# Performance work log

Hardware: AMD Instinct MI355X
Metric: run time of the kernel (lower is better)

## Reference

```python
import math
import jax, jax.numpy as jnp
import numpy as np

LN_EPS = 1e-5
SIG_DOMAIN = 5.0


def _layer_norm(x, gamma, beta):
    mu = jnp.mean(x, axis=-1, keepdims=True)
    var = jnp.var(x, axis=-1, keepdims=True)
    return (x - mu) / jnp.sqrt(var + LN_EPS) * gamma + beta


def setup_inputs() -> dict:
    key = jax.random.key(0)
    k0, k1, k2, k3 = jax.random.split(key, 4)
    B, H, S, D = 4, 16, 1024, 256   # batch, c_heads, seq, input_dim
    A, O = 128, 256                 # attention_dim, output_dim
    x = jax.random.normal(k0, (B, H, S, D), dtype=jnp.float32)
    # torch.rand -> uniform [0,1)
    W_query = jax.random.uniform(k1, (H, A, D), dtype=jnp.float32)
    W_key = jax.random.uniform(k2, (H, A, D), dtype=jnp.float32)
    W_value = jax.random.uniform(k3, (H, O, D), dtype=jnp.float32)
    gamma = jnp.ones((D,), dtype=jnp.float32)
    beta = jnp.zeros((D,), dtype=jnp.float32)
    return {"x": x, "W_query": W_query, "W_key": W_key, "W_value": W_value,
            "gamma": gamma, "beta": beta}


def reference(x, W_query, W_key, W_value, gamma, beta):
    scale = math.sqrt(x.shape[-1])  # sqrt(input_dim)
    xn = _layer_norm(x, gamma, beta)                       # [B,H,S,D]
    q = jnp.einsum('bhsd,had->bhsa', xn, W_query)          # [B,H,S,A]
    k = jnp.einsum('bhsd,had->bhsa', xn, W_key)            # [B,H,S,A]
    v = jnp.einsum('bhsd,hod->bhso', xn, W_value)          # [B,H,S,O]
    scores = jnp.einsum('bhsa,bhta->bhst', q, k) / scale   # [B,H,S,S]
    # overtaking-sigmoid-tuned normalization
    s_max = jnp.max(scores, axis=-1, keepdims=True)
    s_min = jnp.min(scores, axis=-1, keepdims=True)
    s_norm = (scores - s_min) / (s_max - s_min)
    softmax_sel = 1.0 - jax.nn.sigmoid(
        (1.0 - jnp.max(s_norm, axis=-1, keepdims=True)) * 2.0 * SIG_DOMAIN + SIG_DOMAIN)
    sigmoid_sel = 1.0 - softmax_sel
    weights = (softmax_sel * jax.nn.softmax(s_norm, axis=-1)
               + sigmoid_sel * jax.nn.sigmoid(s_norm * 2.0 * SIG_DOMAIN - SIG_DOMAIN))
    return jnp.einsum('bhst,bhto->bhso', weights, v)       # [B,H,S,O]
```

## Files before the change

### kernel.cpp

```cpp
#include <hip/hip_runtime.h>

typedef __attribute__((ext_vector_type(8))) short bf16x8;
typedef __attribute__((ext_vector_type(8))) _Float16 h16x8;
typedef __attribute__((ext_vector_type(2))) _Float16 h16x2;
typedef __attribute__((ext_vector_type(2))) __fp16 fp16x2;
typedef __attribute__((ext_vector_type(4))) float f32x4;
typedef __attribute__((ext_vector_type(4))) unsigned short us4;
typedef unsigned short u16;

#define MFMA16  __builtin_amdgcn_mfma_f32_16x16x32_bf16
#define MFMA16H __builtin_amdgcn_mfma_f32_16x16x32_f16

__device__ __forceinline__ u16 f2bf(float f) {
  union { float f; unsigned u; } v; v.f = f;
  unsigned r = v.u + 0x7FFFu + ((v.u >> 16) & 1u);
  return (u16)(r >> 16);
}

__device__ __forceinline__ float ex2(float x) {
#if __has_builtin(__builtin_amdgcn_exp2f)
  return __builtin_amdgcn_exp2f(x);
#else
  return exp2f(x);
#endif
}

__device__ __forceinline__ h16x8 sigmoid8(h16x8 sv, float am, float bm) {
  h16x8 pa;
  h16x2* pw = (h16x2*)&pa;
  #pragma unroll
  for (int q = 0; q < 4; q++) {
    float e0 = ex2(fmaf((float)sv[2*q],     am, bm));
    float e1 = ex2(fmaf((float)sv[2*q + 1], am, bm));
    fp16x2 pk = __builtin_amdgcn_cvt_pkrtz(__builtin_amdgcn_rcpf(1.0f + e0),
                                           __builtin_amdgcn_rcpf(1.0f + e1));
    pw[q] = __builtin_bit_cast(h16x2, pk);
  }
  return pa;
}

__global__ __launch_bounds__(256) void ln_kernel(const float* __restrict__ x,
    const float* __restrict__ gamma, const float* __restrict__ beta,
    u16* __restrict__ xn)
{
  int row = blockIdx.x * 4 + (threadIdx.x >> 6);
  int lane = threadIdx.x & 63;
  const float* xr = x + (size_t)row * 256;
  f32x4 v = *(const f32x4*)(xr + lane * 4);
  float s  = v[0] + v[1] + v[2] + v[3];
  float s2 = v[0]*v[0] + v[1]*v[1] + v[2]*v[2] + v[3]*v[3];
  #pragma unroll
  for (int off = 1; off < 64; off <<= 1) {
    s  += __shfl_xor(s, off);
    s2 += __shfl_xor(s2, off);
  }
  float mu   = s * (1.0f / 256.0f);
  float var  = s2 * (1.0f / 256.0f) - mu * mu;
  float rstd = rsqrtf(var + 1e-5f);
  f32x4 g  = *(const f32x4*)(gamma + lane * 4);
  f32x4 bb = *(const f32x4*)(beta  + lane * 4);
  us4 o;
  #pragma unroll
  for (int j = 0; j < 4; j++) o[j] = f2bf((v[j] - mu) * rstd * g[j] + bb[j]);
  *(us4*)(xn + (size_t)row * 256 + lane * 4) = o;
}

__global__ __launch_bounds__(256) void cvt_kernel(const float* __restrict__ in,
    u16* __restrict__ out, int n4)
{
  int i = blockIdx.x * 256 + threadIdx.x;
  if (i >= n4) return;
  f32x4 v = *(const f32x4*)(in + (size_t)i * 4);
  us4 o;
  #pragma unroll
  for (int j = 0; j < 4; j++) o[j] = f2bf(v[j]);
  *(us4*)(out + (size_t)i * 4) = o;
}

__global__ __launch_bounds__(256) void cvt_qk(const float* __restrict__ in,
    u16* __restrict__ out, int half)
{
  int i = blockIdx.x * 256 + threadIdx.x;
  int e4 = i * 4;
  int h = e4 >> 15;
  int rem = e4 & 32767;
  f32x4 v = *(const f32x4*)(in + e4);
  us4 o;
  #pragma unroll
  for (int j = 0; j < 4; j++) o[j] = f2bf(v[j]);
  *(us4*)(out + (size_t)h * 65536 + half * 32768 + rem) = o;
}

__global__ __launch_bounds__(256) void gemm128(const u16* __restrict__ Ag,
    const u16* __restrict__ Bg, u16* __restrict__ Cg,
    int M, int N, int aHead, int bHead, int outHalf)
{
  constexpr int K = 256;
  __shared__ u16 As[128][128];
  __shared__ u16 Bs[128][128];
  int bh = blockIdx.z;
  int m0 = blockIdx.x * 128, n0 = blockIdx.y * 128;
  const u16* Ab = Ag + (size_t)(aHead ? (bh & 15) : bh) * M * K + (size_t)m0 * K;
  const u16* Bb = Bg + (size_t)(bHead ? (bh & 15) : bh) * N * K + (size_t)n0 * K;
  int tid = threadIdx.x, lane = tid & 63, w = tid >> 6;
  int wm = w >> 1, wn = w & 1;
  int lr = lane & 15, g = lane >> 4;

  f32x4 acc[4][4] = {};
  for (int kc = 0; kc < 2; kc++) {
    if (kc) __syncthreads();
    #pragma unroll
    for (int i = 0; i < 8; i++) {
      int c = tid + 256 * i;
      int r = c >> 4, ch = c & 15;
      int sw = (ch ^ (r & 7)) * 8;
      *(bf16x8*)&As[r][sw] = *(const bf16x8*)(Ab + (size_t)r * K + kc * 128 + ch * 8);
      *(bf16x8*)&Bs[r][sw] = *(const bf16x8*)(Bb + (size_t)r * K + kc * 128 + ch * 8);
    }
    __syncthreads();
    #pragma unroll
    for (int ks = 0; ks < 4; ks++) {
      bf16x8 af[4], bfr[4];
      #pragma unroll
      for (int mf = 0; mf < 4; mf++) {
        int r = wm * 64 + mf * 16 + lr;
        af[mf] = *(const bf16x8*)&As[r][((ks * 4 + g) ^ (r & 7)) * 8];
      }
      #pragma unroll
      for (int nf = 0; nf < 4; nf++) {
        int r = wn * 64 + nf * 16 + lr;
        bfr[nf] = *(const bf16x8*)&Bs[r][((ks * 4 + g) ^ (r & 7)) * 8];
      }
      #pragma unroll
      for (int mf = 0; mf < 4; mf++)
        #pragma unroll
        for (int nf = 0; nf < 4; nf++)
          acc[mf][nf] = MFMA16(af[mf], bfr[nf], acc[mf][nf], 0, 0, 0);
    }
  }
  u16* Cb = Cg + (size_t)bh * M * N;
  #pragma unroll
  for (int mf = 0; mf < 4; mf++)
    #pragma unroll
    for (int nf = 0; nf < 4; nf++)
      #pragma unroll
      for (int i = 0; i < 4; i++) {
        int row = m0 + wm * 64 + mf * 16 + g * 4 + i;
        int col = n0 + wn * 64 + nf * 16 + lr;
        u16 ev;
        if (outHalf) { _Float16 hv = (_Float16)acc[mf][nf][i]; ev = *(u16*)&hv; }
        else ev = f2bf(acc[mf][nf][i]);
        Cb[(size_t)row * N + col] = ev;
      }
}

__global__ __launch_bounds__(256) void score_kernel(
    const u16* __restrict__ QKg, _Float16* __restrict__ Sg, float2* __restrict__ rp, int bh0)
{
  constexpr int S = 1024, LD = 256;
  __shared__ u16 Qs[128][128];
  __shared__ u16 Ks[128][128];
  int bid = blockIdx.x;
  int hl = ((bid >> 6) << 3) | (bid & 7);
  int rb = (bid >> 3) & 7;
  int bh = bh0 + hl;
  int m0 = rb * 128;
  int tid = threadIdx.x, lane = tid & 63, w = tid >> 6;
  int lr = lane & 15, g = lane >> 4;
  const u16* Qb = QKg + ((size_t)bh * S + m0) * LD;
  const u16* Kb = QKg + (size_t)bh * S * LD + 128;

  #pragma unroll
  for (int i = 0; i < 8; i++) {
    int c = tid + 256 * i;
    int r = c >> 4, ch = c & 15;
    *(bf16x8*)&Qs[r][(ch ^ (r & 7)) * 8] = *(const bf16x8*)(Qb + (size_t)r * LD + ch * 8);
    *(bf16x8*)&Ks[r][(ch ^ (r & 7)) * 8] = *(const bf16x8*)(Kb + (size_t)r * LD + ch * 8);
  }
  __syncthreads();

  bf16x8 aq[2][4];
  #pragma unroll
  for (int mf = 0; mf < 2; mf++)
    #pragma unroll
    for (int ks = 0; ks < 4; ks++) {
      int r = w * 32 + mf * 16 + lr;
      aq[mf][ks] = *(const bf16x8*)&Qs[r][((ks * 4 + g) ^ (r & 7)) * 8];
    }

  float rmin[2][4], rmax[2][4];
  #pragma unroll
  for (int mf = 0; mf < 2; mf++)
    #pragma unroll
    for (int i = 0; i < 4; i++) { rmin[mf][i] = 3.0e38f; rmax[mf][i] = -3.0e38f; }

  _Float16* Sb = Sg + (size_t)hl * S * S;
  for (int nc = 0; nc < 8; nc++) {
    bf16x8 kreg[8];
    if (nc < 7) {
      #pragma unroll
      for (int i = 0; i < 8; i++) {
        int c = tid + 256 * i;
        int r = c >> 4, ch = c & 15;
        kreg[i] = *(const bf16x8*)(Kb + (size_t)(128 * (nc + 1) + r) * LD + ch * 8);
      }
    }
    f32x4 acc[2][8] = {};
    #pragma unroll
    for (int ks = 0; ks < 4; ks++) {
      bf16x8 bk[8];
      #pragma unroll
      for (int nf = 0; nf < 8; nf++) {
        int r = nf * 16 + lr;
        bk[nf] = *(const bf16x8*)&Ks[r][((ks * 4 + g) ^ (r & 7)) * 8];
      }
      #pragma unroll
      for (int mf = 0; mf < 2; mf++)
        #pragma unroll
        for (int nf = 0; nf < 8; nf++)
          acc[mf][nf] = MFMA16(aq[mf][ks], bk[nf], acc[mf][nf], 0, 0, 0);
    }
    #pragma unroll
    for (int mf = 0; mf < 2; mf++)
      #pragma unroll
      for (int nf = 0; nf < 8; nf++) {
        int kt = nc * 4 + (nf >> 1);
        int cc = (nf & 1) * 16 + lr;
        #pragma unroll
        for (int i = 0; i < 4; i++) {
          int rowT = w * 32 + mf * 16 + g * 4 + i;
          int rb64 = (m0 + rowT) >> 6;
          int rr = rowT & 63;
          Sb[(size_t)rb64 * 65536 + (size_t)kt * 2048 + rr * 32 + cc] = (_Float16)acc[mf][nf][i];
          rmin[mf][i] = fminf(rmin[mf][i], acc[mf][nf][i]);
          rmax[mf][i] = fmaxf(rmax[mf][i], acc[mf][nf][i]);
        }
      }
    __syncthreads();
    if (nc < 7) {
      #pragma unroll
      for (int i = 0; i < 8; i++) {
        int c = tid + 256 * i;
        int r = c >> 4, ch = c & 15;
        *(bf16x8*)&Ks[r][(ch ^ (r & 7)) * 8] = kreg[i];
      }
    }
    __syncthreads();
  }
  #pragma unroll
  for (int off = 1; off < 16; off <<= 1)
    #pragma unroll
    for (int mf = 0; mf < 2; mf++)
      #pragma unroll
      for (int i = 0; i < 4; i++) {
        rmin[mf][i] = fminf(rmin[mf][i], __shfl_xor(rmin[mf][i], off));
        rmax[mf][i] = fmaxf(rmax[mf][i], __shfl_xor(rmax[mf][i], off));
      }
  if (lr == 0) {
    #pragma unroll
    for (int mf = 0; mf < 2; mf++)
      #pragma unroll
      for (int i = 0; i < 4; i++) {
        int row = m0 + w * 32 + mf * 16 + g * 4 + i;
        float inv = 1.0f / (rmax[mf][i] - rmin[mf][i]);
        rp[(size_t)bh * S + row] = make_float2(10.0f * inv, fmaf(-10.0f * rmin[mf][i], inv, -5.0f));
      }
  }
}

__global__ __launch_bounds__(256, 4) void pv_kernel(
    const _Float16* __restrict__ Sg, const float2* __restrict__ rpG,
    const _Float16* __restrict__ VTg, float* __restrict__ Out, int bh0)
{
  constexpr int S = 1024, OD = 256, PSTR = 40;
  __shared__ _Float16 P_lds[2][64 * PSTR];
  int bid = blockIdx.x;
  int hl = ((bid >> 7) << 3) | (bid & 7);
  int rb = (bid >> 3) & 15;
  int bh = bh0 + hl;
  int m0 = rb * 64;
  int tid = threadIdx.x, lane = tid & 63, w = tid >> 6;
  int lr = lane & 15, g = lane >> 4;
  const _Float16* Vb = VTg + (size_t)bh * OD * S;

  const _Float16* Stile = Sg + (size_t)hl * S * S + (size_t)rb * 65536 + (size_t)tid * 8;

  int r0 = tid >> 2;
  float2 pp = rpG[(size_t)bh * S + m0 + r0];
  float am = -pp.x * 1.44269504f, bm = -pp.y * 1.44269504f;
  _Float16* Pw0 = &P_lds[0][r0 * PSTR + (tid & 3) * 8];
  _Float16* Pw1 = &P_lds[1][r0 * PSTR + (tid & 3) * 8];

  const _Float16* Vrow[4];
  #pragma unroll
  for (int of = 0; of < 4; of++)
    Vrow[of] = Vb + (size_t)(w * 64 + of * 16 + lr) * S + g * 8;

  f32x4 acc[4][4] = {};

  h16x8 sv0 = *(const h16x8*)(Stile);
  h16x8 sv1 = *(const h16x8*)(Stile + 2048);
  h16x8 va[4], vb[4];
  #pragma unroll
  for (int of = 0; of < 4; of++) va[of] = *(const h16x8*)(Vrow[of]);
  *(h16x8*)Pw0 = sigmoid8(sv0, am, bm);
  __syncthreads();

  for (int kt = 0; kt < 32; kt++) {
    int cur = kt & 1;
    if (kt < 31) {
      #pragma unroll
      for (int of = 0; of < 4; of++)
        vb[of] = *(const h16x8*)(Vrow[of] + (kt + 1) * 32);
    }
    h16x8 svn;
    if (kt < 30) svn = *(const h16x8*)(Stile + (size_t)(kt + 2) * 2048);
    if (kt < 31)
      *(h16x8*)(cur ? Pw0 : Pw1) = sigmoid8(sv1, am, bm);
    __builtin_amdgcn_s_setprio(1);
    #pragma unroll
    for (int rf = 0; rf < 4; rf++) {
      h16x8 pb = *(const h16x8*)&P_lds[cur][(rf * 16 + lr) * PSTR + g * 8];
      #pragma unroll
      for (int of = 0; of < 4; of++)
        acc[of][rf] = MFMA16H(va[of], pb, acc[of][rf], 0, 0, 0);
    }
    __builtin_amdgcn_s_setprio(0);
    #pragma unroll
    for (int of = 0; of < 4; of++) va[of] = vb[of];
    sv0 = sv1; sv1 = svn;
    __syncthreads();
  }

  const float c2 = 0.9933071490757153f;
  float* Ob = Out + (size_t)bh * S * OD;
  #pragma unroll
  for (int of = 0; of < 4; of++)
    #pragma unroll
    for (int rf = 0; rf < 4; rf++) {
      f32x4 v = acc[of][rf];
      #pragma unroll
      for (int i = 0; i < 4; i++) v[i] *= c2;
      int row = m0 + rf * 16 + lr;
      int col = w * 64 + of * 16 + g * 4;
      *(f32x4*)(Ob + (size_t)row * OD + col) = v;
    }
}

extern "C" void kernel_launch(void* const* d_in, const int* in_sizes, int n_in,
                              void* d_out, int out_size, void* d_ws, size_t ws_size,
                              hipStream_t stream) {
  const float* x     = (const float*)d_in[0];
  const float* Wq    = (const float*)d_in[1];
  const float* Wk    = (const float*)d_in[2];
  const float* Wv    = (const float*)d_in[3];
  const float* gamma = (const float*)d_in[4];
  const float* beta  = (const float*)d_in[5];
  float* out = (float*)d_out;

  constexpr int B = 4, H = 16, S = 1024, D = 256, A = 128, O = 256;
  constexpr int BH = B * H;

  char* p = (char*)d_ws;
  size_t off = 0;
  auto take = [&](size_t n) { off = (off + 255) & ~(size_t)255; char* q = p + off; off += n; return q; };

  u16*    xn   = (u16*)take((size_t)BH * S * D * 2);
  u16*    qkb  = (u16*)take((size_t)BH * S * 256 * 2);
  u16*    vtb  = (u16*)take((size_t)BH * O * S * 2);
  u16*    wqkb = (u16*)take((size_t)H * 256 * D * 2);
  u16*    wvb  = (u16*)take((size_t)H * O * D * 2);
  float2* rp   = (float2*)take((size_t)BH * S * 8);

  int grp = 1;
  for (; grp < 8; grp <<= 1) {
    size_t need = ((off + 255) & ~(size_t)255) + (size_t)(BH / grp) * S * S * 2;
    if (need <= ws_size) break;
  }
  int hp = BH / grp;
  _Float16* sG = (_Float16*)take((size_t)hp * S * S * 2);

  ln_kernel<<<BH * S / 4, 256, 0, stream>>>(x, gamma, beta, xn);

  cvt_qk<<<(H * A * D / 4) / 256, 256, 0, stream>>>(Wq, wqkb, 0);
  cvt_qk<<<(H * A * D / 4) / 256, 256, 0, stream>>>(Wk, wqkb, 1);
  cvt_kernel<<<(H * O * D / 4 + 255) / 256, 256, 0, stream>>>(Wv, wvb, H * O * D / 4);

  gemm128<<<dim3(S / 128, 256 / 128, BH), 256, 0, stream>>>(xn, wqkb, qkb, S, 256, 0, 1, 0);
  gemm128<<<dim3(O / 128, S / 128, BH), 256, 0, stream>>>(wvb, xn, vtb, O, S, 1, 0, 1);

  for (int gi = 0; gi < grp; gi++) {
    int bh0 = gi * hp;
    score_kernel<<<hp * 8, 256, 0, stream>>>(qkb, sG, rp, bh0);
    pv_kernel<<<hp * 16, 256, 0, stream>>>((const _Float16*)sG, rp,
                                           (const _Float16*)vtb, out, bh0);
  }
}
```

Before: 190.7 us.

## Restructure PV kernel so each wave owns query rows and skips LDS staging

The PV kernel now gives each wave 16 query rows across all 256 output columns. Each wave computes its own sigmoid weights in registers as the MFMA A operand, so the shared-memory P buffer, the double buffering and the per-iteration barriers are removed. The cost is that every wave reloads the full V tile from global memory (fourfold more V traffic per block) with no explicit prefetch. Output stores become scalar strided writes instead of float4 vectors, and launch bounds drop to 3 blocks per CU.

Result: slower. 352.6 us (+84.9%).

```diff
diff --git a/kernel.cpp b/kernel.cpp
--- a/kernel.cpp
+++ b/kernel.cpp
@@ -268,83 +268,45 @@
   }
 }
 
-__global__ __launch_bounds__(256, 4) void pv_kernel(
+__global__ __launch_bounds__(256, 3) void pv_kernel(
     const _Float16* __restrict__ Sg, const float2* __restrict__ rpG,
     const _Float16* __restrict__ VTg, float* __restrict__ Out, int bh0)
 {
-  constexpr int S = 1024, OD = 256, PSTR = 40;
-  __shared__ _Float16 P_lds[2][64 * PSTR];
+  constexpr int S = 1024, OD = 256;
   int bid = blockIdx.x;
   int hl = ((bid >> 7) << 3) | (bid & 7);
   int rb = (bid >> 3) & 15;
   int bh = bh0 + hl;
-  int m0 = rb * 64;
   int tid = threadIdx.x, lane = tid & 63, w = tid >> 6;
   int lr = lane & 15, g = lane >> 4;
-  const _Float16* Vb = VTg + (size_t)bh * OD * S;
-
-  const _Float16* Stile = Sg + (size_t)hl * S * S + (size_t)rb * 65536 + (size_t)tid * 8;
-
-  int r0 = tid >> 2;
-  float2 pp = rpG[(size_t)bh * S + m0 + r0];
+  int qbase = rb * 64 + w * 16;
+  const _Float16* Vb = VTg + (size_t)bh * OD * S + (size_t)lr * S + g * 8;
+  const _Float16* Sa = Sg + (size_t)hl * S * S + (size_t)rb * 65536
+                     + (w * 16 + lr) * 32 + g * 8;
+  float2 pp = rpG[(size_t)bh * S + qbase + lr];
   float am = -pp.x * 1.44269504f, bm = -pp.y * 1.44269504f;
-  _Float16* Pw0 = &P_lds[0][r0 * PSTR + (tid & 3) * 8];
-  _Float16* Pw1 = &P_lds[1][r0 * PSTR + (tid & 3) * 8];
-
-  const _Float16* Vrow[4];
-  #pragma unroll
-  for (int of = 0; of < 4; of++)
-    Vrow[of] = Vb + (size_t)(w * 64 + of * 16 + lr) * S + g * 8;
-
-  f32x4 acc[4][4] = {};
-
-  h16x8 sv0 = *(const h16x8*)(Stile);
-  h16x8 sv1 = *(const h16x8*)(Stile + 2048);
-  h16x8 va[4], vb[4];
-  #pragma unroll
-  for (int of = 0; of < 4; of++) va[of] = *(const h16x8*)(Vrow[of]);
-  *(h16x8*)Pw0 = sigmoid8(sv0, am, bm);
-  __syncthreads();
-
+
+  f32x4 acc[16] = {};
   for (int kt = 0; kt < 32; kt++) {
-    int cur = kt & 1;
-    if (kt < 31) {
-      #pragma unroll
-      for (int of = 0; of < 4; of++)
-        vb[of] = *(const h16x8*)(Vrow[of] + (kt + 1) * 32);
-    }
-    h16x8 svn;
-    if (kt < 30) svn = *(const h16x8*)(Stile + (size_t)(kt + 2) * 2048);
-    if (kt < 31)
-      *(h16x8*)(cur ? Pw0 : Pw1) = sigmoid8(sv1, am, bm);
+    h16x8 sv = *(const h16x8*)(Sa + (size_t)kt * 2048);
+    h16x8 pa = sigmoid8(sv, am, bm);
+    const _Float16* vp = Vb + kt * 32;
     __builtin_amdgcn_s_setprio(1);
     #pragma unroll
-    for (int rf = 0; rf < 4; rf++) {
-      h16x8 pb = *(const h16x8*)&P_lds[cur][(rf * 16 + lr) * PSTR + g * 8];
-      #pragma unroll
-      for (int of = 0; of < 4; of++)
-        acc[of][rf] = MFMA16H(va[of], pb, acc[of][rf], 0, 0, 0);
+    for (int nf = 0; nf < 16; nf++) {
+      h16x8 bv = *(const h16x8*)(vp + (size_t)(nf * 16) * S);
+      acc[nf] = MFMA16H(pa, bv, acc[nf], 0, 0, 0);
     }
     __builtin_amdgcn_s_setprio(0);
-    #pragma unroll
-    for (int of = 0; of < 4; of++) va[of] = vb[of];
-    sv0 = sv1; sv1 = svn;
-    __syncthreads();
   }
 
   const float c2 = 0.9933071490757153f;
-  float* Ob = Out + (size_t)bh * S * OD;
-  #pragma unroll
-  for (int of = 0; of < 4; of++)
-    #pragma unroll
-    for (int rf = 0; rf < 4; rf++) {
-      f32x4 v = acc[of][rf];
-      #pragma unroll
-      for (int i = 0; i < 4; i++) v[i] *= c2;
-      int row = m0 + rf * 16 + lr;
-      int col = w * 64 + of * 16 + g * 4;
-      *(f32x4*)(Ob + (size_t)row * OD + col) = v;
-    }
+  float* Ob = Out + ((size_t)bh * S + qbase) * OD;
+  #pragma unroll
+  for (int nf = 0; nf < 16; nf++)
+    #pragma unroll
+    for (int i = 0; i < 4; i++)
+      Ob[(size_t)(g * 4 + i) * OD + nf * 16 + lr] = c2 * acc[nf][i];
 }
 
 extern "C" void kernel_launch(void* const* d_in, const int* in_sizes, int n_in,
```
